# Performance work log

Measured on AMD Instinct MI355X. Metric: run time of the kernel, lower is better.

The kernel has to match this reference:

```python
import jax, jax.numpy as jnp
import numpy as np

C = 768
HEADS = 12

def setup_inputs() -> dict:
    key = jax.random.key(0)
    k1, k2, k3 = jax.random.split(key, 3)
    x = jax.random.normal(k1, (8, C, 32, 32), dtype=jnp.float32)
    # 1x1 convs are channel-wise linear maps; store as [out_c, in_c]
    w_qkv = jax.random.normal(k2, (3 * C, C), dtype=jnp.float32) * (C ** -0.5)
    w_proj = jax.random.normal(k3, (C, C), dtype=jnp.float32) * (C ** -0.5)
    return {"x": x, "w_qkv": w_qkv, "w_proj": w_proj}

def reference(x, w_qkv, w_proj):
    b, c, h, w = x.shape
    heads = HEADS
    dh = c // heads
    n = h * w
    scale = dh ** -0.5
    # 1x1 conv QKV: [b, 3c, h, w] -> [b, 3, heads, dh, n]
    qkv = jnp.einsum('oc,bchw->bohw', w_qkv, x).reshape(b, 3, heads, dh, n)
    q, k, v = qkv[:, 0], qkv[:, 1], qkv[:, 2]  # each [b, heads, dh, n]
    attn = jnp.einsum('bhdn,bhdm->bhnm', q, k) * scale  # [b, heads, n, n]
    attn = jax.nn.softmax(attn, axis=-1)
    out = jnp.einsum('bhnm,bhdm->bhdn', attn, v)  # [b, heads, dh, n]
    out = out.reshape(b, c, h, w)
    return jnp.einsum('oc,bchw->bohw', w_proj, out)
```

## Files before the change

kernel.cpp:

```cpp
#include <hip/hip_runtime.h>

typedef unsigned short u16;
typedef unsigned int u32;
typedef float v4f __attribute__((ext_vector_type(4)));
typedef __bf16 bf16x8 __attribute__((ext_vector_type(8)));

#define BATCH 8
#define CDIM 768
#define NHEAD 12
#define DH 64
#define NSEQ 1024
#define SCL 0.18033688011112042f

__device__ __forceinline__ u16 f2bf(float f) {
  u32 u = __builtin_bit_cast(u32, f);
  u += 0x7fffu + ((u >> 16) & 1u);
  return (u16)(u >> 16);
}

__device__ __forceinline__ u16 b16(float f) {
  return (u16)((__builtin_bit_cast(u32, f) + 0x8000u) >> 16);
}

__device__ __forceinline__ u32 pkbf(float hi, float lo) {
  u32 a = __builtin_bit_cast(u32, hi) + 0x8000u;
  u32 b = __builtin_bit_cast(u32, lo) + 0x8000u;
  return __builtin_amdgcn_perm(a, b, 0x07060302u);
}

__device__ __forceinline__ v4f mfma16(bf16x8 a, bf16x8 b, v4f c) {
  return __builtin_amdgcn_mfma_f32_16x16x32_bf16(a, b, c, 0, 0, 0);
}

__device__ __forceinline__ void gload16(const u16* g, u16* l) {
  __builtin_amdgcn_global_load_lds(
      (const __attribute__((address_space(1))) void*)g,
      (__attribute__((address_space(3))) void*)l, 16, 0, 0);
}

#define BARQ asm volatile("s_barrier" ::: "memory")
#define LGKM0 asm volatile("s_waitcnt lgkmcnt(0)" ::: "memory")
#define VMC0 asm volatile("s_waitcnt vmcnt(0)" ::: "memory")
#define FEN asm volatile("" ::: "memory")

__global__ __launch_bounds__(256) void k_prep(const float* __restrict__ x,
                                              const float* __restrict__ wq,
                                              const float* __restrict__ wp,
                                              u16* __restrict__ xT,
                                              u16* __restrict__ wqb,
                                              u16* __restrict__ wpb) {
  __shared__ u16 Ts[64][72];
  int bid = blockIdx.x;
  int t = threadIdx.x;
  if (bid < 2304) {
    bool isQ = bid < 1728;
    const float* s = isQ ? wq : wp;
    u16* d = isQ ? wqb : wpb;
    int i = (isQ ? bid : bid - 1728) * 256 + t;
    float4 v = ((const float4*)s)[i];
    u32 lo = (u32)f2bf(v.x) | ((u32)f2bf(v.y) << 16);
    u32 hi = (u32)f2bf(v.z) | ((u32)f2bf(v.w) << 16);
    ((uint2*)d)[i] = uint2{lo, hi};
    return;
  }
  int id = bid - 2304;
  int p0 = (id & 15) * 64; id >>= 4;
  int c0 = (id % 12) * 64; int b = id / 12;
  int cr = t >> 4;
  int p4 = (t & 15) * 4;
  const float* src = x + ((size_t)b * CDIM + c0) * NSEQ + p0;
#pragma unroll
  for (int i = 0; i < 4; ++i) {
    int c = cr + i * 16;
    float4 v = *(const float4*)&src[(size_t)c * NSEQ + p4];
    Ts[p4 + 0][c] = f2bf(v.x);
    Ts[p4 + 1][c] = f2bf(v.y);
    Ts[p4 + 2][c] = f2bf(v.z);
    Ts[p4 + 3][c] = f2bf(v.w);
  }
  __syncthreads();
  int p = t >> 2;
  int cq = t & 3;
  u16* dst = xT + ((size_t)b * NSEQ + p0 + p) * CDIM + c0;
#pragma unroll
  for (int j = 0; j < 2; ++j) {
    int ch = cq + j * 4;
    *(int4*)&dst[ch * 8] = *(const int4*)&Ts[p][ch * 8];
  }
}

#define NKT 24

__global__ __launch_bounds__(512, 2) void k_gemm_qkv(const u16* __restrict__ Wb,
                                                     const u16* __restrict__ xT,
                                                     u16* __restrict__ qkT,
                                                     u16* __restrict__ vbuf) {
  __shared__ u16 sm[3 * 17408];
  int bid = blockIdx.x;
  int swz = (bid & 7) * 32 + (bid >> 3);
  int oIdx = swz % 8, pIdx = swz / 8;
  int oT = oIdx * 288;
  int pG = pIdx * 256;

  int t = threadIdx.x, lane = t & 63, wid = t >> 6;
  int ln = lane & 15, quad = lane >> 4;
  int wm = wid >> 2, wn = wid & 3;

  int lrow = lane >> 2;
  int scg = ((lane & 3) ^ ((lane >> 3) & 3)) * 8;
  bool roleA = wid < 6;
  int w6 = wid - 6;
  const u16* Asrc = Wb + (size_t)(oT + wid * 48 + lrow) * CDIM + scg;
  const u16* Bsrc = xT + (size_t)(pG + (w6 < 0 ? 0 : w6) * 128 + lrow) * CDIM + scg;
  int ldA = wid * 1536;
  int ldB = 9216 + (w6 < 0 ? 0 : w6) * 4096;

#define STAGEQ(bi, kt) do {                                                \
    u16* bb_ = sm + (bi) * 17408;                                          \
    if (roleA) {                                                           \
      const u16* gp_ = Asrc + (kt) * 32;                                   \
      gload16(gp_, bb_ + ldA);                                             \
      gload16(gp_ + (size_t)16 * CDIM, bb_ + ldA + 512);                   \
      gload16(gp_ + (size_t)32 * CDIM, bb_ + ldA + 1024);                  \
    } else {                                                               \
      const u16* gp_ = Bsrc + (kt) * 32;                                   \
      _Pragma("unroll") for (int i_ = 0; i_ < 8; ++i_)                     \
        gload16(gp_ + (size_t)i_ * 16 * CDIM, bb_ + ldB + i_ * 512);       \
    }                                                                      \
  } while (0)

#define DRAINQ do {                                                        \
    if (roleA) asm volatile("s_waitcnt vmcnt(3)" ::: "memory");            \
    else asm volatile("s_waitcnt vmcnt(8)" ::: "memory");                  \
  } while (0)

  int slot = (quad ^ ((ln >> 1) & 3)) * 8;
  int rAr = (wm * 144 + ln) * 32;
  int rBr = 9216 + (wn * 64 + ln) * 32;

  v4f acc[9][4] = {};

  STAGEQ(0, 0);
  FEN;
  STAGEQ(1, 1);
  DRAINQ;
  BARQ;

  for (int j = 0; j < NKT; ++j) {
    const u16* sb = sm + (j % 3) * 17408;
    int bi2 = (j + 2) % 3;

    if (j < NKT - 2) STAGEQ(bi2, j + 2);
    bf16x8 af[5], bfr[4];
#pragma unroll
    for (int m = 0; m < 5; ++m)
      af[m] = *(const bf16x8*)&sb[rAr + m * 512 + slot];
#pragma unroll
    for (int n = 0; n < 4; ++n)
      bfr[n] = *(const bf16x8*)&sb[rBr + n * 512 + slot];
    BARQ;
    LGKM0;
    __builtin_amdgcn_sched_barrier(0);
    __builtin_amdgcn_s_setprio(1);
#pragma unroll
    for (int m = 0; m < 5; ++m)
#pragma unroll
      for (int n = 0; n < 4; ++n)
        acc[m][n] = mfma16(af[m], bfr[n], acc[m][n]);
    __builtin_amdgcn_s_setprio(0);
    BARQ;

    bf16x8 ag[4];
#pragma unroll
    for (int m = 0; m < 4; ++m)
      ag[m] = *(const bf16x8*)&sb[rAr + (m + 5) * 512 + slot];
    if (j < NKT - 2) DRAINQ;
    else if (j == NKT - 2) VMC0;
    BARQ;
    LGKM0;
    __builtin_amdgcn_sched_barrier(0);
    __builtin_amdgcn_s_setprio(1);
#pragma unroll
    for (int m = 0; m < 4; ++m)
#pragma unroll
      for (int n = 0; n < 4; ++n)
        acc[m + 5][n] = mfma16(ag[m], bfr[n], acc[m + 5][n]);
    __builtin_amdgcn_s_setprio(0);
    BARQ;
  }

#pragma unroll
  for (int m = 0; m < 9; ++m) {
#pragma unroll
    for (int n = 0; n < 4; ++n) {
      int ro = oT + wm * 144 + m * 16 + quad * 4;
      int cp = pG + wn * 64 + n * 16 + ln;
      int b = cp >> 10, p = cp & 1023;
      if (ro < 2 * CDIM) {
        u32 lo = (u32)f2bf(acc[m][n][0]) | ((u32)f2bf(acc[m][n][1]) << 16);
        u32 hi = (u32)f2bf(acc[m][n][2]) | ((u32)f2bf(acc[m][n][3]) << 16);
        *(uint2*)&qkT[((size_t)b * NSEQ + p) * 1536 + ro] = uint2{lo, hi};
      } else {
#pragma unroll
        for (int r = 0; r < 4; ++r)
          vbuf[((size_t)b * CDIM + (ro - 2 * CDIM + r)) * NSEQ + p] =
              f2bf(acc[m][n][r]);
      }
    }
  }
#undef STAGEQ
#undef DRAINQ
}

__global__ __launch_bounds__(256) void k_attn(const u16* __restrict__ qkT,
                                              const u16* __restrict__ vbuf,
                                              u16* __restrict__ attnT) {
  int id = blockIdx.x;
  int b = id & 7;
  int j = id >> 3;
  int h = j % 12;
  int nt0 = (j / 12) * 128;

  int t = threadIdx.x, lane = t & 63, wid = t >> 6;
  int ln = lane & 15, quad = lane >> 4;
  int nbase = nt0 + wid * 32;

  __shared__ u16 Ks[2][64 * 64];
  __shared__ u16 Vs[2][64 * 64];
  __shared__ u16 Pa[4][32 * 64];
  u16* myP = Pa[wid];

  const u16* qbase = qkT + ((size_t)b * NSEQ + nbase) * 1536 + h * DH;
  bf16x8 aq[2][2];
#pragma unroll
  for (int mt = 0; mt < 2; ++mt)
#pragma unroll
    for (int ks = 0; ks < 2; ++ks)
      aq[mt][ks] = *(const bf16x8*)&qbase[(size_t)(mt * 16 + ln) * 1536 + ks * 32 + quad * 8];

  bf16x8 ones;
#pragma unroll
  for (int i = 0; i < 8; ++i) ones[i] = __builtin_bit_cast(__bf16, (u16)0x3F80);

  v4f oacc[2][4] = {};
  v4f lacc[2] = {};

  int sr8 = lane >> 3;
  int sch = ((lane & 7) ^ sr8) * 8;
  const u16* kg0 = qkT + ((size_t)b * NSEQ + wid * 16 + sr8) * 1536 + CDIM + h * DH + sch;
  const u16* vg0 = vbuf + ((size_t)b * CDIM + h * DH + wid * 16 + sr8) * NSEQ + sch;
  int sK = (wid * 16) * 64;

  int sw0 = (quad ^ (ln & 7)) * 8;
  int sw1 = ((4 + quad) ^ (ln & 7)) * 8;
  int e7 = ln & 7;

  gload16(kg0, &Ks[0][sK]);
  gload16(kg0 + (size_t)8 * 1536, &Ks[0][sK + 512]);
  gload16(vg0, &Vs[0][sK]);
  gload16(vg0 + 8 * NSEQ, &Vs[0][sK + 512]);
  __syncthreads();

  for (int s = 0; s < 16; ++s) {
    int cur = s & 1, nxt = cur ^ 1;
    if (s < 15) {
      size_t ko = (size_t)(s + 1) * 64 * 1536;
      int vo = (s + 1) * 64;
      gload16(kg0 + ko, &Ks[nxt][sK]);
      gload16(kg0 + ko + (size_t)8 * 1536, &Ks[nxt][sK + 512]);
      gload16(vg0 + vo, &Vs[nxt][sK]);
      gload16(vg0 + vo + 8 * NSEQ, &Vs[nxt][sK + 512]);
    }

#pragma unroll
    for (int ct = 0; ct < 4; ++ct) {
      bf16x8 kf0 = *(const bf16x8*)&Ks[cur][(ct * 16 + ln) * 64 + sw0];
      bf16x8 kf1 = *(const bf16x8*)&Ks[cur][(ct * 16 + ln) * 64 + sw1];
#pragma unroll
      for (int mt = 0; mt < 2; ++mt) {
        v4f sc = {};
        __builtin_amdgcn_s_setprio(1);
        sc = mfma16(kf0, aq[mt][0], sc);
        sc = mfma16(kf1, aq[mt][1], sc);
        __builtin_amdgcn_s_setprio(0);
        float p0 = __builtin_amdgcn_exp2f(sc[0] * SCL);
        float p1 = __builtin_amdgcn_exp2f(sc[1] * SCL);
        float p2 = __builtin_amdgcn_exp2f(sc[2] * SCL);
        float p3 = __builtin_amdgcn_exp2f(sc[3] * SCL);
        int woff = (mt * 16 + ln) * 64 +
                   (((2 * ct + (quad >> 1)) ^ e7) * 8 + (quad & 1) * 4);
        *(uint2*)&myP[woff] = uint2{pkbf(p1, p0), pkbf(p3, p2)};
      }
    }

    bf16x8 ap[2][2];
#pragma unroll
    for (int mt = 0; mt < 2; ++mt)
#pragma unroll
      for (int ks = 0; ks < 2; ++ks)
        ap[mt][ks] = *(const bf16x8*)&myP[(mt * 16 + ln) * 64 +
                                          ((ks * 4 + quad) ^ e7) * 8];
    __builtin_amdgcn_s_setprio(1);
#pragma unroll
    for (int mt = 0; mt < 2; ++mt) {
      lacc[mt] = mfma16(ap[mt][0], ones, lacc[mt]);
      lacc[mt] = mfma16(ap[mt][1], ones, lacc[mt]);
    }
    __builtin_amdgcn_s_setprio(0);
#pragma unroll
    for (int nt = 0; nt < 4; ++nt) {
      bf16x8 vf0 = *(const bf16x8*)&Vs[cur][(nt * 16 + ln) * 64 + sw0];
      bf16x8 vf1 = *(const bf16x8*)&Vs[cur][(nt * 16 + ln) * 64 + sw1];
      __builtin_amdgcn_s_setprio(1);
#pragma unroll
      for (int mt = 0; mt < 2; ++mt) {
        oacc[mt][nt] = mfma16(ap[mt][0], vf0, oacc[mt][nt]);
        oacc[mt][nt] = mfma16(ap[mt][1], vf1, oacc[mt][nt]);
      }
      __builtin_amdgcn_s_setprio(0);
    }
    __syncthreads();
  }

#pragma unroll
  for (int mt = 0; mt < 2; ++mt) {
#pragma unroll
    for (int r = 0; r < 4; ++r) {
      float inv = 1.0f / lacc[mt][r];
      int n = nbase + mt * 16 + quad * 4 + r;
      u16* dst = attnT + ((size_t)b * NSEQ + n) * CDIM + h * DH;
#pragma unroll
      for (int nt = 0; nt < 4; ++nt)
        dst[nt * 16 + ln] = b16(oacc[mt][nt][r] * inv);
    }
  }
}

__global__ __launch_bounds__(256, 2) void k_gemm_proj(const u16* __restrict__ Wb,
                                                      const u16* __restrict__ aT,
                                                      float* __restrict__ out) {
  __shared__ u16 sm[3 * 10240];
  int bid = blockIdx.x;
  int swz = (bid & 7) * 32 + (bid >> 3);
  int oIdx = swz % 4, pIdx = swz / 4;
  int oT = oIdx * 192;
  int pG = pIdx * 128;

  int t = threadIdx.x, lane = t & 63, wid = t >> 6;
  int ln = lane & 15, quad = lane >> 4;
  int wm = wid >> 1, wn = wid & 1;

  int lrow = lane >> 2;
  int scg = ((lane & 3) ^ ((lane >> 3) & 3)) * 8;
  bool roleA = wid < 3;
  const u16* Asrc = Wb + (size_t)(oT + wid * 64 + lrow) * CDIM + scg;
  const u16* Bsrc = aT + (size_t)(pG + lrow) * CDIM + scg;
  int ldA = wid * 2048;
  int ldB = 6144;

#define STAGEP(bi, kt) do {                                                \
    u16* bb_ = sm + (bi) * 10240;                                          \
    if (roleA) {                                                           \
      const u16* gp_ = Asrc + (kt) * 32;                                   \
      _Pragma("unroll") for (int i_ = 0; i_ < 4; ++i_)                     \
        gload16(gp_ + (size_t)i_ * 16 * CDIM, bb_ + ldA + i_ * 512);       \
    } else {                                                               \
      const u16* gp_ = Bsrc + (kt) * 32;                                   \
      _Pragma("unroll") for (int i_ = 0; i_ < 8; ++i_)                     \
        gload16(gp_ + (size_t)i_ * 16 * CDIM, bb_ + ldB + i_ * 512);       \
    }                                                                      \
  } while (0)

#define DRAINP do {                                                        \
    if (roleA) asm volatile("s_waitcnt vmcnt(4)" ::: "memory");            \
    else asm volatile("s_waitcnt vmcnt(8)" ::: "memory");                  \
  } while (0)

  int slot = (quad ^ ((ln >> 1) & 3)) * 8;
  int rAr = (wm * 96 + ln) * 32;
  int rBr = 6144 + (wn * 64 + ln) * 32;

  v4f acc[6][4] = {};

  STAGEP(0, 0);
  FEN;
  STAGEP(1, 1);
  DRAINP;
  BARQ;

  for (int j = 0; j < NKT; ++j) {
    const u16* sb = sm + (j % 3) * 10240;
    int bi2 = (j + 2) % 3;

    if (j < NKT - 2) STAGEP(bi2, j + 2);
    bf16x8 af[3], bfr[4];
#pragma unroll
    for (int m = 0; m < 3; ++m)
      af[m] = *(const bf16x8*)&sb[rAr + m * 512 + slot];
#pragma unroll
    for (int n = 0; n < 4; ++n)
      bfr[n] = *(const bf16x8*)&sb[rBr + n * 512 + slot];
    BARQ;
    LGKM0;
    __builtin_amdgcn_sched_barrier(0);
    __builtin_amdgcn_s_setprio(1);
#pragma unroll
    for (int m = 0; m < 3; ++m)
#pragma unroll
      for (int n = 0; n < 4; ++n)
        acc[m][n] = mfma16(af[m], bfr[n], acc[m][n]);
    __builtin_amdgcn_s_setprio(0);
    BARQ;

    bf16x8 ag[3];
#pragma unroll
    for (int m = 0; m < 3; ++m)
      ag[m] = *(const bf16x8*)&sb[rAr + (m + 3) * 512 + slot];
    if (j < NKT - 2) DRAINP;
    else if (j == NKT - 2) VMC0;
    BARQ;
    LGKM0;
    __builtin_amdgcn_sched_barrier(0);
    __builtin_amdgcn_s_setprio(1);
#pragma unroll
    for (int m = 0; m < 3; ++m)
#pragma unroll
      for (int n = 0; n < 4; ++n)
        acc[m + 3][n] = mfma16(ag[m], bfr[n], acc[m + 3][n]);
    __builtin_amdgcn_s_setprio(0);
    BARQ;
  }

#pragma unroll
  for (int m = 0; m < 6; ++m) {
#pragma unroll
    for (int n = 0; n < 4; ++n) {
      int ro = oT + wm * 96 + m * 16 + quad * 4;
      int cp = pG + wn * 64 + n * 16 + ln;
      int b = cp >> 10, p = cp & 1023;
#pragma unroll
      for (int r = 0; r < 4; ++r)
        out[((size_t)b * CDIM + ro + r) * NSEQ + p] = acc[m][n][r];
    }
  }
#undef STAGEP
#undef DRAINP
}

extern "C" void kernel_launch(void* const* d_in, const int* in_sizes, int n_in,
                              void* d_out, int out_size, void* d_ws, size_t ws_size,
                              hipStream_t stream) {
  const float* x = (const float*)d_in[0];
  const float* w_qkv = (const float*)d_in[1];
  const float* w_proj = (const float*)d_in[2];
  float* out = (float*)d_out;

  char* ws = (char*)d_ws;
  u16* wqkv_bf = (u16*)(ws);
  u16* wproj_bf = (u16*)(ws + 3538944);
  u16* xT = (u16*)(ws + 4718592);
  u16* vbuf = (u16*)(ws + 17301504);
  u16* qkT = (u16*)d_out;
  u16* attnT = xT;

  k_prep<<<dim3(3840), dim3(256), 0, stream>>>(x, w_qkv, w_proj, xT, wqkv_bf, wproj_bf);
  k_gemm_qkv<<<dim3(256), dim3(512), 0, stream>>>(wqkv_bf, xT, qkT, vbuf);
  k_attn<<<dim3(768), dim3(256), 0, stream>>>(qkT, vbuf, attnT);
  k_gemm_proj<<<dim3(256), dim3(256), 0, stream>>>(wproj_bf, attnT, out);
}
```

Baseline: 176.6 us.

## Software-pipeline attention loop: overlap next tile's QK/exp with current PV

Restructures the attention inner loop into a two-tile unrolled pipeline. The QK^T scores and exp of tile s+1 are computed and their P fragments read into registers before the PV MFMAs of tile s run. K and V loads are now staged separately, each on its own schedule. The aim is to hide exp/VALU latency and LDS round-trips behind matrix work, at the cost of more live registers for the second P fragment set. It also drops the priority hints around the QK MFMAs.

```diff
diff --git a/kernel.cpp b/kernel.cpp
--- a/kernel.cpp
+++ b/kernel.cpp
@@ -249,78 +249,96 @@
   int sch = ((lane & 7) ^ sr8) * 8;
   const u16* kg0 = qkT + ((size_t)b * NSEQ + wid * 16 + sr8) * 1536 + CDIM + h * DH + sch;
   const u16* vg0 = vbuf + ((size_t)b * CDIM + h * DH + wid * 16 + sr8) * NSEQ + sch;
-  int sK = (wid * 16) * 64;
+  int sK = wid * 1024;
 
   int sw0 = (quad ^ (ln & 7)) * 8;
   int sw1 = ((4 + quad) ^ (ln & 7)) * 8;
   int e7 = ln & 7;
 
-  gload16(kg0, &Ks[0][sK]);
-  gload16(kg0 + (size_t)8 * 1536, &Ks[0][sK + 512]);
-  gload16(vg0, &Vs[0][sK]);
-  gload16(vg0 + 8 * NSEQ, &Vs[0][sK + 512]);
+#define STAGEK(kb, s_) do { size_t ko_ = (size_t)(s_) * 64 * 1536;          \
+    gload16(kg0 + ko_, &Ks[kb][sK]);                                        \
+    gload16(kg0 + ko_ + (size_t)8 * 1536, &Ks[kb][sK + 512]); } while (0)
+#define STAGEV(vb, s_) do { int vo_ = (s_) * 64;                            \
+    gload16(vg0 + vo_, &Vs[vb][sK]);                                        \
+    gload16(vg0 + vo_ + 8 * NSEQ, &Vs[vb][sK + 512]); } while (0)
+
+#define QKEXP(kb) do {                                                      \
+    _Pragma("unroll") for (int ct = 0; ct < 4; ++ct) {                      \
+      bf16x8 kf0 = *(const bf16x8*)&Ks[kb][(ct * 16 + ln) * 64 + sw0];      \
+      bf16x8 kf1 = *(const bf16x8*)&Ks[kb][(ct * 16 + ln) * 64 + sw1];      \
+      _Pragma("unroll") for (int mt = 0; mt < 2; ++mt) {                    \
+        v4f sc = {};                                                        \
+        sc = mfma16(kf0, aq[mt][0], sc);                                    \
+        sc = mfma16(kf1, aq[mt][1], sc);                                    \
+        float p0 = __builtin_amdgcn_exp2f(sc[0] * SCL);                     \
+        float p1 = __builtin_amdgcn_exp2f(sc[1] * SCL);                     \
+        float p2 = __builtin_amdgcn_exp2f(sc[2] * SCL);                     \
+        float p3 = __builtin_amdgcn_exp2f(sc[3] * SCL);                     \
+        int woff = (mt * 16 + ln) * 64 +                                    \
+                   (((2 * ct + (quad >> 1)) ^ e7) * 8 + (quad & 1) * 4);    \
+        *(uint2*)&myP[woff] = uint2{pkbf(p1, p0), pkbf(p3, p2)};            \
+      }                                                                     \
+    }                                                                       \
+  } while (0)
+
+#define READAP(ap) do {                                                     \
+    _Pragma("unroll") for (int mt = 0; mt < 2; ++mt)                        \
+      _Pragma("unroll") for (int ks = 0; ks < 2; ++ks)                      \
+        ap[mt][ks] = *(const bf16x8*)&myP[(mt * 16 + ln) * 64 +             \
+                                          ((ks * 4 + quad) ^ e7) * 8];      \
+  } while (0)
+
+#define PVSTEP(vb, ap) do {                                                 \
+    __builtin_amdgcn_s_setprio(1);                                          \
+    _Pragma("unroll") for (int mt = 0; mt < 2; ++mt) {                      \
+      lacc[mt] = mfma16(ap[mt][0], ones, lacc[mt]);                         \
+      lacc[mt] = mfma16(ap[mt][1], ones, lacc[mt]);                         \
+    }                                                                       \
+    __builtin_amdgcn_s_setprio(0);                                          \
+    _Pragma("unroll") for (int nt = 0; nt < 4; ++nt) {                      \
+      bf16x8 vf0 = *(const bf16x8*)&Vs[vb][(nt * 16 + ln) * 64 + sw0];      \
+      bf16x8 vf1 = *(const bf16x8*)&Vs[vb][(nt * 16 + ln) * 64 + sw1];      \
+      __builtin_amdgcn_s_setprio(1);                                        \
+      _Pragma("unroll") for (int mt = 0; mt < 2; ++mt) {                    \
+        oacc[mt][nt] = mfma16(ap[mt][0], vf0, oacc[mt][nt]);                \
+        oacc[mt][nt] = mfma16(ap[mt][1], vf1, oacc[mt][nt]);                \
+      }                                                                     \
+      __builtin_amdgcn_s_setprio(0);                                        \
+    }                                                                       \
+  } while (0)
+
+  bf16x8 apA[2][2], apB[2][2];
+
+  STAGEK(0, 0);
+  STAGEV(0, 0);
   __syncthreads();
-
-  for (int s = 0; s < 16; ++s) {
-    int cur = s & 1, nxt = cur ^ 1;
-    if (s < 15) {
-      size_t ko = (size_t)(s + 1) * 64 * 1536;
-      int vo = (s + 1) * 64;
-      gload16(kg0 + ko, &Ks[nxt][sK]);
-      gload16(kg0 + ko + (size_t)8 * 1536, &Ks[nxt][sK + 512]);
-      gload16(vg0 + vo, &Vs[nxt][sK]);
-      gload16(vg0 + vo + 8 * NSEQ, &Vs[nxt][sK + 512]);
+  QKEXP(0);
+  STAGEK(1, 1);
+  READAP(apA);
+
+#pragma unroll 1
+  for (int s = 0; s < 16; s += 2) {
+    __syncthreads();
+    if (s < 14) STAGEK(0, s + 2);
+    STAGEV(1, s + 1);
+    QKEXP(1);
+    PVSTEP(0, apA);
+    READAP(apB);
+    __syncthreads();
+    if (s < 13) STAGEK(1, s + 3);
+    if (s < 14) {
+      STAGEV(0, s + 2);
+      QKEXP(0);
     }
-
-#pragma unroll
-    for (int ct = 0; ct < 4; ++ct) {
-      bf16x8 kf0 = *(const bf16x8*)&Ks[cur][(ct * 16 + ln) * 64 + sw0];
-      bf16x8 kf1 = *(const bf16x8*)&Ks[cur][(ct * 16 + ln) * 64 + sw1];
-#pragma unroll
-      for (int mt = 0; mt < 2; ++mt) {
-        v4f sc = {};
-        __builtin_amdgcn_s_setprio(1);
-        sc = mfma16(kf0, aq[mt][0], sc);
-        sc = mfma16(kf1, aq[mt][1], sc);
-        __builtin_amdgcn_s_setprio(0);
-        float p0 = __builtin_amdgcn_exp2f(sc[0] * SCL);
-        float p1 = __builtin_amdgcn_exp2f(sc[1] * SCL);
-        float p2 = __builtin_amdgcn_exp2f(sc[2] * SCL);
-        float p3 = __builtin_amdgcn_exp2f(sc[3] * SCL);
-        int woff = (mt * 16 + ln) * 64 +
-                   (((2 * ct + (quad >> 1)) ^ e7) * 8 + (quad & 1) * 4);
-        *(uint2*)&myP[woff] = uint2{pkbf(p1, p0), pkbf(p3, p2)};
-      }
-    }
-
-    bf16x8 ap[2][2];
-#pragma unroll
-    for (int mt = 0; mt < 2; ++mt)
-#pragma unroll
-      for (int ks = 0; ks < 2; ++ks)
-        ap[mt][ks] = *(const bf16x8*)&myP[(mt * 16 + ln) * 64 +
-                                          ((ks * 4 + quad) ^ e7) * 8];
-    __builtin_amdgcn_s_setprio(1);
-#pragma unroll
-    for (int mt = 0; mt < 2; ++mt) {
-      lacc[mt] = mfma16(ap[mt][0], ones, lacc[mt]);
-      lacc[mt] = mfma16(ap[mt][1], ones, lacc[mt]);
-    }
-    __builtin_amdgcn_s_setprio(0);
-#pragma unroll
-    for (int nt = 0; nt < 4; ++nt) {
-      bf16x8 vf0 = *(const bf16x8*)&Vs[cur][(nt * 16 + ln) * 64 + sw0];
-      bf16x8 vf1 = *(const bf16x8*)&Vs[cur][(nt * 16 + ln) * 64 + sw1];
-      __builtin_amdgcn_s_setprio(1);
-#pragma unroll
-      for (int mt = 0; mt < 2; ++mt) {
-        oacc[mt][nt] = mfma16(ap[mt][0], vf0, oacc[mt][nt]);
-        oacc[mt][nt] = mfma16(ap[mt][1], vf1, oacc[mt][nt]);
-      }
-      __builtin_amdgcn_s_setprio(0);
-    }
-    __syncthreads();
-  }
+    PVSTEP(1, apB);
+    if (s < 14) READAP(apA);
+  }
+
+#undef STAGEK
+#undef STAGEV
+#undef QKEXP
+#undef READAP
+#undef PVSTEP
 
 #pragma unroll
   for (int mt = 0; mt < 2; ++mt) {
```

After: 172.4 us. 1.02x faster.
